# Performance work log

Hardware: AMD Instinct MI355X
Metric: run time of the kernel (lower is better)

## Reference

```python
import jax, jax.numpy as jnp
import numpy as np

N_NODES = 50000
N_EDGES = 640000
IN_FEAT = 128
H_FEAT = 128
OUT_FEAT = 128
N_CLASSES = 16
BN_EPS = 1e-5


def gcn_conv(x, W, b, edge_index, n_nodes):
    """PyG GCNConv: add self-loops, symmetric deg^{-1/2} normalization,
    gather -> weighted message -> scatter_add, plus bias."""
    loop = jnp.arange(n_nodes, dtype=edge_index.dtype)
    src = jnp.concatenate([edge_index[0], loop])  # [E+N]
    dst = jnp.concatenate([edge_index[1], loop])  # [E+N]
    ones = jnp.ones(src.shape[0], dtype=x.dtype)
    deg = jax.ops.segment_sum(ones, dst, num_segments=n_nodes)  # >=1 (self loops)
    dinv = jax.lax.rsqrt(deg)
    norm = dinv[src] * dinv[dst]  # [E+N]
    h = x @ W  # [N, F_out]
    msgs = h[src] * norm[:, None]  # gather + scale, [E+N, F_out]
    out = jax.ops.segment_sum(msgs, dst, num_segments=n_nodes)  # scatter_add
    return out + b


def setup_inputs() -> dict:
    key = jax.random.key(0)
    ks = jax.random.split(key, 10)
    seq = jax.random.normal(ks[0], (N_NODES, IN_FEAT), dtype=jnp.float32)
    edge_index = jax.random.randint(ks[1], (2, N_EDGES), 0, N_NODES, dtype=jnp.int64)
    s1 = 1.0 / np.sqrt(IN_FEAT)
    s2 = 1.0 / np.sqrt(H_FEAT)
    s3 = 1.0 / np.sqrt(OUT_FEAT)
    W1 = jax.random.uniform(ks[2], (IN_FEAT, H_FEAT), jnp.float32, -s1, s1)
    b1 = jnp.zeros((H_FEAT,), jnp.float32)
    gamma = jnp.ones((H_FEAT,), jnp.float32)
    beta = jnp.zeros((H_FEAT,), jnp.float32)
    running_mean = 0.1 * jax.random.normal(ks[3], (H_FEAT,), jnp.float32)
    running_var = jax.random.uniform(ks[4], (H_FEAT,), jnp.float32, 0.5, 1.5)
    W2 = jax.random.uniform(ks[5], (H_FEAT, OUT_FEAT), jnp.float32, -s2, s2)
    b2 = jnp.zeros((OUT_FEAT,), jnp.float32)
    Wc = jax.random.uniform(ks[6], (OUT_FEAT, N_CLASSES), jnp.float32, -s3, s3)
    bc = jax.random.uniform(ks[7], (N_CLASSES,), jnp.float32, -s3, s3)
    return {
        "seq": seq, "edge_index": edge_index,
        "W1": W1, "b1": b1, "gamma": gamma, "beta": beta,
        "running_mean": running_mean, "running_var": running_var,
        "W2": W2, "b2": b2, "Wc": Wc, "bc": bc,
    }


def reference(seq, edge_index, W1, b1, gamma, beta, running_mean, running_var, W2, b2, Wc, bc):
    # inference mode: BN uses running stats, dropout is identity
    n = seq.shape[0]
    h = gcn_conv(seq, W1, b1, edge_index, n)
    h = (h - running_mean) * jax.lax.rsqrt(running_var + BN_EPS) * gamma + beta
    h = jax.nn.relu(h)
    h = gcn_conv(h, W2, b2, edge_index, n)
    return h @ Wc + bc
```

## Files before the change

### kernel.cpp

```cpp
#include <hip/hip_runtime.h>
#include <math.h>

#define N_NODES 50000
#define N_EDGES 640000
#define FDIM 128
#define NCLS 16
#define BN_EPS 1e-5f
#define NBG 391
#define NBF 625
#define ELLW 64

typedef __attribute__((ext_vector_type(8))) short bf16x8;
typedef __attribute__((ext_vector_type(4))) float f32x4;

__device__ __forceinline__ unsigned pack_bf16x2(float lo, float hi) {
    unsigned ul = __float_as_uint(lo);
    unsigned uh = __float_as_uint(hi);
    ul += 0x7fff + ((ul >> 16) & 1);
    uh += 0x7fff + ((uh >> 16) & 1);
    return (ul >> 16) | (uh & 0xffff0000u);
}
__device__ __forceinline__ unsigned short bf16_rne(float x) {
    unsigned u = __float_as_uint(x);
    u += 0x7fff + ((u >> 16) & 1);
    return (unsigned short)(u >> 16);
}
__device__ __forceinline__ float bf_lo(unsigned u) { return __uint_as_float(u << 16); }
__device__ __forceinline__ float bf_hi(unsigned u) { return __uint_as_float(u & 0xffff0000u); }

__device__ __forceinline__ void async_copy16(const void* g, void* l) {
    __builtin_amdgcn_global_load_lds(
        (const __attribute__((address_space(1))) unsigned*)g,
        (__attribute__((address_space(3))) unsigned*)l, 16, 0, 0);
}

__global__ __launch_bounds__(256) void pack_fold_zero_kernel(
        const float* __restrict__ W1, const float* __restrict__ W2,
        const float* __restrict__ Wc, const float* __restrict__ b1,
        const float* __restrict__ b2, const float* __restrict__ bc,
        const float* __restrict__ gamma, const float* __restrict__ beta,
        const float* __restrict__ rmean, const float* __restrict__ rvar,
        bf16x8* __restrict__ WPK,
        float* __restrict__ W2c, float* __restrict__ bc2, float4* __restrict__ fusedq,
        uint4* __restrict__ degz) {
    int tid = threadIdx.x;
    int bid = blockIdx.x;

    {
        int gz = bid * 256 + tid;
#pragma unroll
        for (int i = 0; i < 4; i++) {
            int idx = gz + i * 4096;
            if (idx < 12544) degz[idx] = make_uint4(0, 0, 0, 0);
        }
    }

    if (bid >= 8) {
        int fi = (bid - 8) * 256 + tid;
        int lane = fi & 63, kt = (fi >> 6) & 3, ct = fi >> 8;
        int kbase = kt * 32 + (lane >> 4) * 8;
        int col = ct * 16 + (lane & 15);
        short h[8], lo[8];
#pragma unroll
        for (int j = 0; j < 8; j++) {
            float wv = W1[(kbase + j) * 128 + col];
            unsigned short hs = bf16_rne(wv);
            float rem = wv - __uint_as_float(((unsigned)hs) << 16);
            h[j] = (short)hs;
            lo[j] = (short)bf16_rne(rem);
        }
        WPK[fi] = *(bf16x8*)h;
        WPK[2048 + fi] = *(bf16x8*)lo;
    } else {
        int gid = bid * 256 + tid;
        int r = gid >> 4, c = gid & 15;
        float acc = 0.f;
#pragma unroll 8
        for (int k = 0; k < 128; k++) acc += W2[r * 128 + k] * Wc[k * 16 + c];
        W2c[gid] = acc;
        if (bid == 0) {
            if (tid < 16) {
                float a = bc[tid];
                for (int k = 0; k < 128; k++) a += b2[k] * Wc[k * 16 + tid];
                bc2[tid] = a;
            }
            if (tid < 64) {
                int c0 = tid * 2, c1 = c0 + 1;
                float sc0 = gamma[c0] * rsqrtf(rvar[c0] + BN_EPS);
                float sc1 = gamma[c1] * rsqrtf(rvar[c1] + BN_EPS);
                float sh0 = (b1[c0] - rmean[c0]) * sc0 + beta[c0];
                float sh1 = (b1[c1] - rmean[c1]) * sc1 + beta[c1];
                fusedq[tid] = make_float4(sc0, sh0, sc1, sh1);
            }
        }
    }
}

__global__ __launch_bounds__(256) void gemm_fill_kernel(
        const float* __restrict__ seq, const bf16x8* __restrict__ WPK,
        unsigned* __restrict__ bufA,
        const int* __restrict__ eidx, int* __restrict__ deg, int* __restrict__ ell) {
    __shared__ __align__(16) char smem[65536];
    int tid = threadIdx.x;
    int bid = blockIdx.x;

    if (bid >= NBF) {
        int gb = bid - NBF;
        int w = tid >> 6, l = tid & 63;

        {
            const char* gsrc = (const char*)WPK;
#pragma unroll
            for (int r = 0; r < 16; r++)
                async_copy16(gsrc + (size_t)(r * 256 + tid) * 16,
                             smem + (r * 4 + w) * 1024);
        }

        int la = l & 15, q = l >> 4;
        int rb = gb * 128 + w * 16;
        int arow0 = rb + la;
        int arow1 = rb + 64 + la;
        bool ok0 = arow0 < N_NODES, ok1 = arow1 < N_NODES;
        const float4* X4 = (const float4*)seq;

        float4 xr0[8], xr1[8];
        float4 z4 = make_float4(0.f, 0.f, 0.f, 0.f);
#pragma unroll
        for (int kt = 0; kt < 4; kt++) {
            xr0[kt * 2]     = ok0 ? X4[arow0 * 32 + kt * 8 + q * 2]     : z4;
            xr0[kt * 2 + 1] = ok0 ? X4[arow0 * 32 + kt * 8 + q * 2 + 1] : z4;
            xr1[kt * 2]     = ok1 ? X4[arow1 * 32 + kt * 8 + q * 2]     : z4;
            xr1[kt * 2 + 1] = ok1 ? X4[arow1 * 32 + kt * 8 + q * 2 + 1] : z4;
        }
        bf16x8 ah0[4], al0[4], ah1[4], al1[4];
#pragma unroll
        for (int kt = 0; kt < 4; kt++) {
            const float* xv0 = (const float*)&xr0[kt * 2];
            const float* xv1 = (const float*)&xr1[kt * 2];
#pragma unroll
            for (int j = 0; j < 8; j++) {
                float v = xv0[j];
                unsigned short hs = bf16_rne(v);
                ah0[kt][j] = (short)hs;
                al0[kt][j] = (short)bf16_rne(v - __uint_as_float(((unsigned)hs) << 16));
                float u = xv1[j];
                unsigned short hs1 = bf16_rne(u);
                ah1[kt][j] = (short)hs1;
                al1[kt][j] = (short)bf16_rne(u - __uint_as_float(((unsigned)hs1) << 16));
            }
        }
        f32x4 acc0[8], acc1[8];
#pragma unroll
        for (int ct = 0; ct < 8; ct++) {
            acc0[ct] = (f32x4){0.f, 0.f, 0.f, 0.f};
            acc1[ct] = (f32x4){0.f, 0.f, 0.f, 0.f};
        }

        __syncthreads();

        const bf16x8* WH = (const bf16x8*)smem;
        const bf16x8* WL = (const bf16x8*)(smem + 32768);
#pragma unroll
        for (int kt = 0; kt < 4; kt++) {
#pragma unroll
            for (int ct = 0; ct < 8; ct++) {
                bf16x8 bh = WH[(ct * 4 + kt) * 64 + l];
                bf16x8 bl = WL[(ct * 4 + kt) * 64 + l];
                acc0[ct] = __builtin_amdgcn_mfma_f32_16x16x32_bf16(bh, ah0[kt], acc0[ct], 0, 0, 0);
                acc1[ct] = __builtin_amdgcn_mfma_f32_16x16x32_bf16(bh, ah1[kt], acc1[ct], 0, 0, 0);
                acc0[ct] = __builtin_amdgcn_mfma_f32_16x16x32_bf16(bl, ah0[kt], acc0[ct], 0, 0, 0);
                acc1[ct] = __builtin_amdgcn_mfma_f32_16x16x32_bf16(bl, ah1[kt], acc1[ct], 0, 0, 0);
                acc0[ct] = __builtin_amdgcn_mfma_f32_16x16x32_bf16(bh, al0[kt], acc0[ct], 0, 0, 0);
                acc1[ct] = __builtin_amdgcn_mfma_f32_16x16x32_bf16(bh, al1[kt], acc1[ct], 0, 0, 0);
            }
        }

        if (ok0) {
            unsigned* dp = bufA + (size_t)arow0 * 64 + q * 2;
#pragma unroll
            for (int ct = 0; ct < 8; ct++) {
                uint2 u;
                u.x = pack_bf16x2(acc0[ct][0], acc0[ct][1]);
                u.y = pack_bf16x2(acc0[ct][2], acc0[ct][3]);
                *(uint2*)(dp + ct * 8) = u;
            }
        }
        if (ok1) {
            unsigned* dp = bufA + (size_t)arow1 * 64 + q * 2;
#pragma unroll
            for (int ct = 0; ct < 8; ct++) {
                uint2 u;
                u.x = pack_bf16x2(acc1[ct][0], acc1[ct][1]);
                u.y = pack_bf16x2(acc1[ct][2], acc1[ct][3]);
                *(uint2*)(dp + ct * 8) = u;
            }
        }
    } else {
        const int4* src4 = (const int4*)eidx;
        const int4* dst4 = (const int4*)(eidx + N_EDGES);
        int t = bid * 256 + tid;
        int4 sv = src4[t];
        int4 dv = dst4[t];
        {
            int s = atomicAdd(&deg[dv.x], 1);
            if (s < ELLW) ell[dv.x * ELLW + s] = sv.x;
        }
        {
            int s = atomicAdd(&deg[dv.y], 1);
            if (s < ELLW) ell[dv.y * ELLW + s] = sv.y;
        }
        {
            int s = atomicAdd(&deg[dv.z], 1);
            if (s < ELLW) ell[dv.z * ELLW + s] = sv.z;
        }
        {
            int s = atomicAdd(&deg[dv.w], 1);
            if (s < ELLW) ell[dv.w * ELLW + s] = sv.w;
        }
    }
}

__global__ __launch_bounds__(256) void agg1_kernel(const unsigned* __restrict__ Hb,
                                                   const int* __restrict__ ell,
                                                   const int* __restrict__ deg,
                                                   const float4* __restrict__ fusedq,
                                                   const float* __restrict__ W2c,
                                                   float* __restrict__ Z) {
    __shared__ float sH[4][128];
    int w = threadIdx.x >> 6, l = threadIdx.x & 63;
    int node = blockIdx.x * 4 + w;
    int dgt = __builtin_amdgcn_readfirstlane(deg[node]);
    int dg = dgt < ELLW ? dgt : ELLW;
    float di = rsqrtf((float)(dgt + 1));
    const int* row = ell + node * ELLW;

    int s_l = (l < dg) ? row[l] : 0;
    float w_l = (l < dg) ? rsqrtf((float)(deg[s_l] + 1)) * di : 0.f;

    int c = l & 15, q = l >> 4;
    float wreg[32];
#pragma unroll
    for (int i = 0; i < 32; i++) wreg[i] = W2c[(q * 32 + i) * 16 + c];

    unsigned hv = Hb[(size_t)node * 64 + l];
    float n2 = di * di;
    float acc0 = bf_lo(hv) * n2, acc1 = bf_hi(hv) * n2;

    int dgr = (dg + 7) & ~7;
    for (int e = 0; e < dgr; e += 8) {
        int t0 = __shfl(s_l, e + 0), t1 = __shfl(s_l, e + 1);
        int t2 = __shfl(s_l, e + 2), t3 = __shfl(s_l, e + 3);
        int t4 = __shfl(s_l, e + 4), t5 = __shfl(s_l, e + 5);
        int t6 = __shfl(s_l, e + 6), t7 = __shfl(s_l, e + 7);
        float x0 = __shfl(w_l, e + 0), x1 = __shfl(w_l, e + 1);
        float x2 = __shfl(w_l, e + 2), x3 = __shfl(w_l, e + 3);
        float x4 = __shfl(w_l, e + 4), x5 = __shfl(w_l, e + 5);
        float x6 = __shfl(w_l, e + 6), x7 = __shfl(w_l, e + 7);
        unsigned u0 = Hb[(size_t)t0 * 64 + l];
        unsigned u1 = Hb[(size_t)t1 * 64 + l];
        unsigned u2 = Hb[(size_t)t2 * 64 + l];
        unsigned u3 = Hb[(size_t)t3 * 64 + l];
        unsigned u4 = Hb[(size_t)t4 * 64 + l];
        unsigned u5 = Hb[(size_t)t5 * 64 + l];
        unsigned u6 = Hb[(size_t)t6 * 64 + l];
        unsigned u7 = Hb[(size_t)t7 * 64 + l];
        acc0 += bf_lo(u0) * x0 + bf_lo(u1) * x1 + bf_lo(u2) * x2 + bf_lo(u3) * x3
              + bf_lo(u4) * x4 + bf_lo(u5) * x5 + bf_lo(u6) * x6 + bf_lo(u7) * x7;
        acc1 += bf_hi(u0) * x0 + bf_hi(u1) * x1 + bf_hi(u2) * x2 + bf_hi(u3) * x3
              + bf_hi(u4) * x4 + bf_hi(u5) * x5 + bf_hi(u6) * x6 + bf_hi(u7) * x7;
    }

    float4 qv = fusedq[l];
    float a0 = fmaxf(acc0 * qv.x + qv.y, 0.f);
    float a1 = fmaxf(acc1 * qv.z + qv.w, 0.f);

    ((float2*)sH[w])[l] = make_float2(a0, a1);
    float z = 0.f;
    const float4* row4 = (const float4*)&sH[w][q * 32];
#pragma unroll
    for (int i = 0; i < 8; i++) {
        float4 v = row4[i];
        z += v.x * wreg[i * 4] + v.y * wreg[i * 4 + 1]
           + v.z * wreg[i * 4 + 2] + v.w * wreg[i * 4 + 3];
    }
    z += __shfl_xor(z, 16);
    z += __shfl_xor(z, 32);
    if (l < 16) Z[(size_t)node * NCLS + l] = z;
}

__global__ __launch_bounds__(256) void agg2_kernel(const float* __restrict__ Z,
                                                   const int* __restrict__ ell,
                                                   const int* __restrict__ deg,
                                                   const float* __restrict__ bc2,
                                                   float* __restrict__ out) {
    int tid = threadIdx.x;
    int c = tid & 15;
    int node = blockIdx.x * 16 + (tid >> 4);
    int lane = tid & 63;
    int baseln = lane & 48;
    int dgt = deg[node];
    int dg = dgt < ELLW ? dgt : ELLW;
    float di = rsqrtf((float)(dgt + 1));
    const int* row = ell + node * ELLW;

    int s0_ = (c < dg) ? row[c] : 0;
    int s1_ = (c + 16 < dg) ? row[c + 16] : 0;
    float w0_ = (c < dg) ? rsqrtf((float)(deg[s0_] + 1)) * di : 0.f;
    float w1_ = (c + 16 < dg) ? rsqrtf((float)(deg[s1_] + 1)) * di : 0.f;
    int s2_ = 0, s3_ = 0;
    float w2_ = 0.f, w3_ = 0.f;
    if (__any(dg > 32)) {
        s2_ = (c + 32 < dg) ? row[c + 32] : 0;
        s3_ = (c + 48 < dg) ? row[c + 48] : 0;
        w2_ = (c + 32 < dg) ? rsqrtf((float)(deg[s2_] + 1)) * di : 0.f;
        w3_ = (c + 48 < dg) ? rsqrtf((float)(deg[s3_] + 1)) * di : 0.f;
    }

    float acc = Z[(size_t)node * NCLS + c] * di * di;

#define A2_BATCH(SS, WW, OFF)                                                        \
    {                                                                                \
        int t0 = __shfl(SS, baseln + OFF + 0), t1 = __shfl(SS, baseln + OFF + 1);    \
        int t2 = __shfl(SS, baseln + OFF + 2), t3 = __shfl(SS, baseln + OFF + 3);    \
        int t4 = __shfl(SS, baseln + OFF + 4), t5 = __shfl(SS, baseln + OFF + 5);    \
        int t6 = __shfl(SS, baseln + OFF + 6), t7 = __shfl(SS, baseln + OFF + 7);    \
        float x0 = __shfl(WW, baseln + OFF + 0), x1 = __shfl(WW, baseln + OFF + 1);  \
        float x2 = __shfl(WW, baseln + OFF + 2), x3 = __shfl(WW, baseln + OFF + 3);  \
        float x4 = __shfl(WW, baseln + OFF + 4), x5 = __shfl(WW, baseln + OFF + 5);  \
        float x6 = __shfl(WW, baseln + OFF + 6), x7 = __shfl(WW, baseln + OFF + 7);  \
        float v0 = Z[(size_t)t0 * NCLS + c];                                         \
        float v1 = Z[(size_t)t1 * NCLS + c];                                         \
        float v2 = Z[(size_t)t2 * NCLS + c];                                         \
        float v3 = Z[(size_t)t3 * NCLS + c];                                         \
        float v4 = Z[(size_t)t4 * NCLS + c];                                         \
        float v5 = Z[(size_t)t5 * NCLS + c];                                         \
        float v6 = Z[(size_t)t6 * NCLS + c];                                         \
        float v7 = Z[(size_t)t7 * NCLS + c];                                         \
        acc += v0 * x0 + v1 * x1 + v2 * x2 + v3 * x3                                 \
             + v4 * x4 + v5 * x5 + v6 * x6 + v7 * x7;                                \
    }

    if (dg > 0)  A2_BATCH(s0_, w0_, 0)
    if (dg > 8)  A2_BATCH(s0_, w0_, 8)
    if (dg > 16) A2_BATCH(s1_, w1_, 0)
    if (dg > 24) A2_BATCH(s1_, w1_, 8)
    if (dg > 32) A2_BATCH(s2_, w2_, 0)
    if (dg > 40) A2_BATCH(s2_, w2_, 8)
    if (dg > 48) A2_BATCH(s3_, w3_, 0)
    if (dg > 56) A2_BATCH(s3_, w3_, 8)
#undef A2_BATCH

    out[(size_t)node * NCLS + c] = acc + bc2[c];
}

extern "C" void kernel_launch(void* const* d_in, const int* in_sizes, int n_in,
                              void* d_out, int out_size, void* d_ws, size_t ws_size,
                              hipStream_t stream) {
    const float* seq   = (const float*)d_in[0];
    const int*   eidx  = (const int*)d_in[1];
    const float* W1    = (const float*)d_in[2];
    const float* b1    = (const float*)d_in[3];
    const float* gamma = (const float*)d_in[4];
    const float* beta  = (const float*)d_in[5];
    const float* rmean = (const float*)d_in[6];
    const float* rvar  = (const float*)d_in[7];
    const float* W2    = (const float*)d_in[8];
    const float* b2    = (const float*)d_in[9];
    const float* Wc    = (const float*)d_in[10];
    const float* bc    = (const float*)d_in[11];

    char* ws = (char*)d_ws;
    size_t off = 0;
    auto alloc = [&](size_t bytes) -> void* {
        void* p = ws + off;
        off = (off + bytes + 255) & ~(size_t)255;
        return p;
    };
    int*    deg      = (int*)alloc(50176 * 4);
    int*    ell      = (int*)alloc((size_t)N_NODES * ELLW * 4);
    float*  W2c      = (float*)alloc(FDIM * NCLS * 4);
    float*  bc2      = (float*)alloc(NCLS * 4);
    float4* fusedq   = (float4*)alloc(64 * 16);
    unsigned* bufA   = (unsigned*)alloc((size_t)N_NODES * (FDIM / 2) * 4);
    float*  Zbuf     = (float*)alloc((size_t)N_NODES * NCLS * 4);
    bf16x8* WPK      = (bf16x8*)alloc(4096 * 16);

    pack_fold_zero_kernel<<<16, 256, 0, stream>>>(
        W1, W2, Wc, b1, b2, bc, gamma, beta, rmean, rvar, WPK, W2c, bc2, fusedq,
        (uint4*)deg);
    gemm_fill_kernel<<<NBF + NBG, 256, 0, stream>>>(seq, WPK, bufA, eidx, deg, ell);
    agg1_kernel<<<N_NODES / 4, 256, 0, stream>>>(bufA, ell, deg, fusedq, W2c, Zbuf);
    agg2_kernel<<<N_NODES / 16, 256, 0, stream>>>(Zbuf, ell, deg, bc2, (float*)d_out);
}
```

Baseline: 186.3 us.

## Merge ELL fill work into GEMM blocks instead of separate fill blocks

```diff
diff --git a/kernel.cpp b/kernel.cpp
--- a/kernel.cpp
+++ b/kernel.cpp
@@ -7,7 +7,7 @@
 #define NCLS 16
 #define BN_EPS 1e-5f
 #define NBG 391
-#define NBF 625
+#define ESTRIDE (NBG * 256)
 #define ELLW 64
 
 typedef __attribute__((ext_vector_type(8))) short bf16x8;
@@ -102,120 +102,110 @@
         const int* __restrict__ eidx, int* __restrict__ deg, int* __restrict__ ell) {
     __shared__ __align__(16) char smem[65536];
     int tid = threadIdx.x;
-    int bid = blockIdx.x;
-
-    if (bid >= NBF) {
-        int gb = bid - NBF;
-        int w = tid >> 6, l = tid & 63;
-
-        {
-            const char* gsrc = (const char*)WPK;
-#pragma unroll
-            for (int r = 0; r < 16; r++)
-                async_copy16(gsrc + (size_t)(r * 256 + tid) * 16,
-                             smem + (r * 4 + w) * 1024);
-        }
-
-        int la = l & 15, q = l >> 4;
-        int rb = gb * 128 + w * 16;
-        int arow0 = rb + la;
-        int arow1 = rb + 64 + la;
-        bool ok0 = arow0 < N_NODES, ok1 = arow1 < N_NODES;
-        const float4* X4 = (const float4*)seq;
-
-        float4 xr0[8], xr1[8];
-        float4 z4 = make_float4(0.f, 0.f, 0.f, 0.f);
-#pragma unroll
-        for (int kt = 0; kt < 4; kt++) {
-            xr0[kt * 2]     = ok0 ? X4[arow0 * 32 + kt * 8 + q * 2]     : z4;
-            xr0[kt * 2 + 1] = ok0 ? X4[arow0 * 32 + kt * 8 + q * 2 + 1] : z4;
-            xr1[kt * 2]     = ok1 ? X4[arow1 * 32 + kt * 8 + q * 2]     : z4;
-            xr1[kt * 2 + 1] = ok1 ? X4[arow1 * 32 + kt * 8 + q * 2 + 1] : z4;
-        }
-        bf16x8 ah0[4], al0[4], ah1[4], al1[4];
-#pragma unroll
-        for (int kt = 0; kt < 4; kt++) {
-            const float* xv0 = (const float*)&xr0[kt * 2];
-            const float* xv1 = (const float*)&xr1[kt * 2];
-#pragma unroll
-            for (int j = 0; j < 8; j++) {
-                float v = xv0[j];
-                unsigned short hs = bf16_rne(v);
-                ah0[kt][j] = (short)hs;
-                al0[kt][j] = (short)bf16_rne(v - __uint_as_float(((unsigned)hs) << 16));
-                float u = xv1[j];
-                unsigned short hs1 = bf16_rne(u);
-                ah1[kt][j] = (short)hs1;
-                al1[kt][j] = (short)bf16_rne(u - __uint_as_float(((unsigned)hs1) << 16));
+    int gb = blockIdx.x;
+    int w = tid >> 6, l = tid & 63;
+
+    {
+        const char* gsrc = (const char*)WPK;
+#pragma unroll
+        for (int r = 0; r < 16; r++)
+            async_copy16(gsrc + (size_t)(r * 256 + tid) * 16,
+                         smem + (r * 4 + w) * 1024);
+    }
+
+    int la = l & 15, q = l >> 4;
+    int rb = gb * 128 + w * 16;
+    int arow0 = rb + la;
+    int arow1 = rb + 64 + la;
+    bool ok0 = arow0 < N_NODES, ok1 = arow1 < N_NODES;
+    const float4* X4 = (const float4*)seq;
+
+    float4 xr0[8], xr1[8];
+    float4 z4 = make_float4(0.f, 0.f, 0.f, 0.f);
+#pragma unroll
+    for (int kt = 0; kt < 4; kt++) {
+        xr0[kt * 2]     = ok0 ? X4[arow0 * 32 + kt * 8 + q * 2]     : z4;
+        xr0[kt * 2 + 1] = ok0 ? X4[arow0 * 32 + kt * 8 + q * 2 + 1] : z4;
+        xr1[kt * 2]     = ok1 ? X4[arow1 * 32 + kt * 8 + q * 2]     : z4;
+        xr1[kt * 2 + 1] = ok1 ? X4[arow1 * 32 + kt * 8 + q * 2 + 1] : z4;
+    }
+    bf16x8 ah0[4], al0[4], ah1[4], al1[4];
+#pragma unroll
+    for (int kt = 0; kt < 4; kt++) {
+        const float* xv0 = (const float*)&xr0[kt * 2];
+        const float* xv1 = (const float*)&xr1[kt * 2];
+#pragma unroll
+        for (int j = 0; j < 8; j++) {
+            float v = xv0[j];
+            unsigned short hs = bf16_rne(v);
+            ah0[kt][j] = (short)hs;
+            al0[kt][j] = (short)bf16_rne(v - __uint_as_float(((unsigned)hs) << 16));
+            float u = xv1[j];
+            unsigned short hs1 = bf16_rne(u);
+            ah1[kt][j] = (short)hs1;
+            al1[kt][j] = (short)bf16_rne(u - __uint_as_float(((unsigned)hs1) << 16));
+        }
+    }
+    f32x4 acc0[8], acc1[8];
+#pragma unroll
+    for (int ct = 0; ct < 8; ct++) {
+        acc0[ct] = (f32x4){0.f, 0.f, 0.f, 0.f};
+        acc1[ct] = (f32x4){0.f, 0.f, 0.f, 0.f};
+    }
+
+    __syncthreads();
+
+    const bf16x8* WH = (const bf16x8*)smem;
+    const bf16x8* WL = (const bf16x8*)(smem + 32768);
+#pragma unroll
+    for (int kt = 0; kt < 4; kt++) {
+#pragma unroll
+        for (int ct = 0; ct < 8; ct++) {
+            bf16x8 bh = WH[(ct * 4 + kt) * 64 + l];
+            bf16x8 bl = WL[(ct * 4 + kt) * 64 + l];
+            acc0[ct] = __builtin_amdgcn_mfma_f32_16x16x32_bf16(bh, ah0[kt], acc0[ct], 0, 0, 0);
+            acc1[ct] = __builtin_amdgcn_mfma_f32_16x16x32_bf16(bh, ah1[kt], acc1[ct], 0, 0, 0);
+            acc0[ct] = __builtin_amdgcn_mfma_f32_16x16x32_bf16(bl, ah0[kt], acc0[ct], 0, 0, 0);
+            acc1[ct] = __builtin_amdgcn_mfma_f32_16x16x32_bf16(bl, ah1[kt], acc1[ct], 0, 0, 0);
+            acc0[ct] = __builtin_amdgcn_mfma_f32_16x16x32_bf16(bh, al0[kt], acc0[ct], 0, 0, 0);
+            acc1[ct] = __builtin_amdgcn_mfma_f32_16x16x32_bf16(bh, al1[kt], acc1[ct], 0, 0, 0);
+        }
+    }
+
+    if (ok0) {
+        unsigned* dp = bufA + (size_t)arow0 * 64 + q * 2;
+#pragma unroll
+        for (int ct = 0; ct < 8; ct++) {
+            uint2 u;
+            u.x = pack_bf16x2(acc0[ct][0], acc0[ct][1]);
+            u.y = pack_bf16x2(acc0[ct][2], acc0[ct][3]);
+            *(uint2*)(dp + ct * 8) = u;
+        }
+    }
+    if (ok1) {
+        unsigned* dp = bufA + (size_t)arow1 * 64 + q * 2;
+#pragma unroll
+        for (int ct = 0; ct < 8; ct++) {
+            uint2 u;
+            u.x = pack_bf16x2(acc1[ct][0], acc1[ct][1]);
+            u.y = pack_bf16x2(acc1[ct][2], acc1[ct][3]);
+            *(uint2*)(dp + ct * 8) = u;
+        }
+    }
+
+    {
+        const int* srcp = eidx;
+        const int* dstp = eidx + N_EDGES;
+        int gtid = gb * 256 + tid;
+#pragma unroll
+        for (int k = 0; k < 7; k++) {
+            int e = gtid + k * ESTRIDE;
+            if (e < N_EDGES) {
+                int sv = srcp[e];
+                int dv = dstp[e];
+                int s = atomicAdd(&deg[dv], 1);
+                if (s < ELLW) ell[dv * ELLW + s] = sv;
             }
-        }
-        f32x4 acc0[8], acc1[8];
-#pragma unroll
-        for (int ct = 0; ct < 8; ct++) {
-            acc0[ct] = (f32x4){0.f, 0.f, 0.f, 0.f};
-            acc1[ct] = (f32x4){0.f, 0.f, 0.f, 0.f};
-        }
-
-        __syncthreads();
-
-        const bf16x8* WH = (const bf16x8*)smem;
-        const bf16x8* WL = (const bf16x8*)(smem + 32768);
-#pragma unroll
-        for (int kt = 0; kt < 4; kt++) {
-#pragma unroll
-            for (int ct = 0; ct < 8; ct++) {
-                bf16x8 bh = WH[(ct * 4 + kt) * 64 + l];
-                bf16x8 bl = WL[(ct * 4 + kt) * 64 + l];
-                acc0[ct] = __builtin_amdgcn_mfma_f32_16x16x32_bf16(bh, ah0[kt], acc0[ct], 0, 0, 0);
-                acc1[ct] = __builtin_amdgcn_mfma_f32_16x16x32_bf16(bh, ah1[kt], acc1[ct], 0, 0, 0);
-                acc0[ct] = __builtin_amdgcn_mfma_f32_16x16x32_bf16(bl, ah0[kt], acc0[ct], 0, 0, 0);
-                acc1[ct] = __builtin_amdgcn_mfma_f32_16x16x32_bf16(bl, ah1[kt], acc1[ct], 0, 0, 0);
-                acc0[ct] = __builtin_amdgcn_mfma_f32_16x16x32_bf16(bh, al0[kt], acc0[ct], 0, 0, 0);
-                acc1[ct] = __builtin_amdgcn_mfma_f32_16x16x32_bf16(bh, al1[kt], acc1[ct], 0, 0, 0);
-            }
-        }
-
-        if (ok0) {
-            unsigned* dp = bufA + (size_t)arow0 * 64 + q * 2;
-#pragma unroll
-            for (int ct = 0; ct < 8; ct++) {
-                uint2 u;
-                u.x = pack_bf16x2(acc0[ct][0], acc0[ct][1]);
-                u.y = pack_bf16x2(acc0[ct][2], acc0[ct][3]);
-                *(uint2*)(dp + ct * 8) = u;
-            }
-        }
-        if (ok1) {
-            unsigned* dp = bufA + (size_t)arow1 * 64 + q * 2;
-#pragma unroll
-            for (int ct = 0; ct < 8; ct++) {
-                uint2 u;
-                u.x = pack_bf16x2(acc1[ct][0], acc1[ct][1]);
-                u.y = pack_bf16x2(acc1[ct][2], acc1[ct][3]);
-                *(uint2*)(dp + ct * 8) = u;
-            }
-        }
-    } else {
-        const int4* src4 = (const int4*)eidx;
-        const int4* dst4 = (const int4*)(eidx + N_EDGES);
-        int t = bid * 256 + tid;
-        int4 sv = src4[t];
-        int4 dv = dst4[t];
-        {
-            int s = atomicAdd(&deg[dv.x], 1);
-            if (s < ELLW) ell[dv.x * ELLW + s] = sv.x;
-        }
-        {
-            int s = atomicAdd(&deg[dv.y], 1);
-            if (s < ELLW) ell[dv.y * ELLW + s] = sv.y;
-        }
-        {
-            int s = atomicAdd(&deg[dv.z], 1);
-            if (s < ELLW) ell[dv.z * ELLW + s] = sv.z;
-        }
-        {
-            int s = atomicAdd(&deg[dv.w], 1);
-            if (s < ELLW) ell[dv.w * ELLW + s] = sv.w;
         }
     }
 }
@@ -388,7 +378,7 @@
     pack_fold_zero_kernel<<<16, 256, 0, stream>>>(
         W1, W2, Wc, b1, b2, bc, gamma, beta, rmean, rvar, WPK, W2c, bc2, fusedq,
         (uint4*)deg);
-    gemm_fill_kernel<<<NBF + NBG, 256, 0, stream>>>(seq, WPK, bufA, eidx, deg, ell);
+    gemm_fill_kernel<<<NBG, 256, 0, stream>>>(seq, WPK, bufA, eidx, deg, ell);
     agg1_kernel<<<N_NODES / 4, 256, 0, stream>>>(bufA, ell, deg, fusedq, W2c, Zbuf);
     agg2_kernel<<<N_NODES / 16, 256, 0, stream>>>(Zbuf, ell, deg, bc2, (float*)d_out);
 }
```

New measurement: 189.0 us. About the same (+1.4%).
